# Kernel optimization log

Measured on AMD Instinct MI355X. Metric: run time of the kernel, lower is better.

The kernel has to match this reference:

```python
import jax, jax.numpy as jnp
import numpy as np


def setup_inputs() -> dict:
    key = jax.random.key(0)
    k1, k2, k3 = jax.random.split(key, 3)
    N, H, K, E = 16384, 1024, 8, 64
    x = jax.random.normal(k1, (N, H), dtype=jnp.float32)
    expert_idx = jax.random.randint(k2, (N, K), 0, E, dtype=jnp.int32)
    scale = jax.random.uniform(k3, (N,), dtype=jnp.float32)
    return {"x": x, "expert_idx": expert_idx, "scale": scale, "expert_num": E}


def reference(x, expert_idx, scale, expert_num):
    # MoE init routing v2, dropless (drop_pad_mode=0), no quant (quant_mode=0),
    # expert_tokens_num_type=0 -> cumulative counts over [0, expert_num).
    N, K = expert_idx.shape
    NK = N * K
    flat_expert = expert_idx.reshape(NK)
    # stable sort by expert id: all (token, k) slots for expert 0 first, etc.
    sort_idx = jnp.argsort(flat_expert, stable=True)          # [N*K]
    token_rows = sort_idx // K                                 # source token per expanded row
    expanded_x = x[token_rows]                                 # [N*K, H] gather
    # inverse permutation: expanded_row_idx[n*K + k] = position in expanded_x
    expanded_row_idx = jnp.zeros((NK,), dtype=jnp.int32).at[sort_idx].set(
        jnp.arange(NK, dtype=jnp.int32))
    # per-expert token counts -> cumulative sum
    counts = jax.ops.segment_sum(jnp.ones((NK,), dtype=jnp.int64),
                                 flat_expert, num_segments=expert_num)
    expert_token_cumsum = jnp.cumsum(counts)                   # [expert_num]
    expanded_scale = scale[token_rows]                         # [N*K]
    return (expanded_x, expanded_row_idx, expert_token_cumsum, expanded_scale)
```

## Files before the change

kernel.cpp:

```cpp
#include <hip/hip_runtime.h>

#define TPB 256

typedef float f32x4 __attribute__((ext_vector_type(4)));

__global__ void k_hist(const int* __restrict__ eidx, int* __restrict__ blockHist,
                       int NK, int E) {
    __shared__ int hist[256];
    int tid = threadIdx.x;
    for (int e = tid; e < E; e += TPB) hist[e] = 0;
    __syncthreads();
    int j = blockIdx.x * TPB + tid;
    if (j < NK) atomicAdd(&hist[eidx[j]], 1);
    __syncthreads();
    for (int e = tid; e < E; e += TPB)
        blockHist[(size_t)blockIdx.x * E + e] = hist[e];
}

__global__ void k_scan_blocks(int* __restrict__ blockHist, int* __restrict__ counts,
                              int numBlocks, int E) {
    __shared__ int s[TPB];
    int e = blockIdx.x;
    int tid = threadIdx.x;
    int per = (numBlocks + TPB - 1) / TPB;
    int start = tid * per;
    int end = start + per; if (end > numBlocks) end = numBlocks;
    int sum = 0;
    for (int b = start; b < end; ++b) sum += blockHist[(size_t)b * E + e];
    s[tid] = sum;
    __syncthreads();
    for (int off = 1; off < TPB; off <<= 1) {
        int t = (tid >= off) ? s[tid - off] : 0;
        __syncthreads();
        s[tid] += t;
        __syncthreads();
    }
    int run = (tid == 0) ? 0 : s[tid - 1];
    if (tid == TPB - 1) counts[e] = s[tid];
    for (int b = start; b < end; ++b) {
        size_t idx = (size_t)b * E + e;
        int v = blockHist[idx];
        blockHist[idx] = run;
        run += v;
    }
}

__global__ void k_scan_experts(const int* __restrict__ counts, int* __restrict__ offsets,
                               float* __restrict__ cumsum_out, int E) {
    if (threadIdx.x == 0) {
        int run = 0;
        for (int e = 0; e < E; ++e) {
            offsets[e] = run;
            run += counts[e];
            cumsum_out[e] = (float)run;
        }
    }
}

__global__ void k_pos(const int* __restrict__ eidx, const float* __restrict__ scale,
                      const int* __restrict__ blockHist, const int* __restrict__ offsets,
                      float* __restrict__ row_idx_out, float* __restrict__ scale_out,
                      int* __restrict__ dstPos, int NK, int E, int K) {
    __shared__ unsigned short se[TPB];
    int tid = threadIdx.x;
    int j = blockIdx.x * TPB + tid;
    int e = 0xFFFF;
    if (j < NK) e = eidx[j];
    se[tid] = (unsigned short)e;
    __syncthreads();
    if (j < NK) {
        unsigned short me = (unsigned short)e;
        int rank = 0;
        for (int t = 0; t < tid; ++t)
            rank += (se[t] == me) ? 1 : 0;
        int pos = offsets[e] + blockHist[(size_t)blockIdx.x * E + e] + rank;
        row_idx_out[j] = (float)pos;
        dstPos[j] = pos;
        scale_out[pos] = scale[j / K];
    }
}

__global__ void k_scatter(const float* __restrict__ x, const int* __restrict__ dstPos,
                          float* __restrict__ out, int H, int K, int N) {
    __shared__ int pos_s[32];
    int n4 = H >> 2;
    int tok = blockIdx.x;
    if (tok >= N) return;
    if (threadIdx.x < K) pos_s[threadIdx.x] = dstPos[tok * K + threadIdx.x];
    __syncthreads();
    const f32x4* xs = (const f32x4*)(x + (size_t)tok * H);
    for (int t = threadIdx.x; t < n4; t += blockDim.x) {
        f32x4 v = xs[t];
        #pragma unroll
        for (int k = 0; k < 8; ++k) {
            if (k < K) {
                f32x4* od = (f32x4*)(out + (size_t)pos_s[k] * H);
                __builtin_nontemporal_store(v, od + t);
            }
        }
    }
}

extern "C" void kernel_launch(void* const* d_in, const int* in_sizes, int n_in,
                              void* d_out, int out_size, void* d_ws, size_t ws_size,
                              hipStream_t stream) {
    const float* x     = (const float*)d_in[0];
    const int*   eidx  = (const int*)d_in[1];
    const float* scale = (const float*)d_in[2];

    const int N  = in_sizes[2];
    const int H  = in_sizes[0] / N;
    const int K  = in_sizes[1] / N;
    const int NK = N * K;
    const int E  = out_size - (int)((long long)NK * H) - 2 * NK;

    const int numBlocks = (NK + TPB - 1) / TPB;

    float* out_x     = (float*)d_out;
    float* out_rowix = out_x + (size_t)NK * H;
    float* out_cum   = out_rowix + NK;
    float* out_scale = out_cum + E;

    int* blockHist = (int*)d_ws;
    int* counts    = blockHist + (size_t)numBlocks * E;
    int* offsets   = counts + E;
    int* dstPos    = offsets + E;

    k_hist<<<numBlocks, TPB, 0, stream>>>(eidx, blockHist, NK, E);
    k_scan_blocks<<<E, TPB, 0, stream>>>(blockHist, counts, numBlocks, E);
    k_scan_experts<<<1, 64, 0, stream>>>(counts, offsets, out_cum, E);
    k_pos<<<numBlocks, TPB, 0, stream>>>(eidx, scale, blockHist, offsets,
                                         out_rowix, out_scale, dstPos, NK, E, K);
    k_scatter<<<N, TPB, 0, stream>>>(x, dstPos, out_x, H, K, N);
}
```

Measured before the change: 127.4 us.

## Fuse position and scatter kernels, single-block global scan, ballot-based ranking

```diff
diff --git a/kernel.cpp b/kernel.cpp
--- a/kernel.cpp
+++ b/kernel.cpp
@@ -17,85 +17,117 @@
         blockHist[(size_t)blockIdx.x * E + e] = hist[e];
 }
 
-__global__ void k_scan_blocks(int* __restrict__ blockHist, int* __restrict__ counts,
-                              int numBlocks, int E) {
-    __shared__ int s[TPB];
-    int e = blockIdx.x;
-    int tid = threadIdx.x;
-    int per = (numBlocks + TPB - 1) / TPB;
-    int start = tid * per;
-    int end = start + per; if (end > numBlocks) end = numBlocks;
+__global__ void k_scan_all(int* __restrict__ blockHist, float* __restrict__ cumsum_out,
+                           int numBlocks, int E, int CH) {
+    __shared__ int s[1024];
+    int t = threadIdx.x;
+    int nT = E * CH;
+    int e = t / CH, c = t % CH;
+    int per = (numBlocks + CH - 1) / CH;
+    int b0 = c * per;
+    int b1 = b0 + per; if (b1 > numBlocks) b1 = numBlocks;
     int sum = 0;
-    for (int b = start; b < end; ++b) sum += blockHist[(size_t)b * E + e];
-    s[tid] = sum;
+    if (t < nT)
+        for (int b = b0; b < b1; ++b) sum += blockHist[(size_t)b * E + e];
+    s[t] = (t < nT) ? sum : 0;
     __syncthreads();
-    for (int off = 1; off < TPB; off <<= 1) {
-        int t = (tid >= off) ? s[tid - off] : 0;
+    for (int off = 1; off < 1024; off <<= 1) {
+        int v = (t >= off) ? s[t - off] : 0;
         __syncthreads();
-        s[tid] += t;
+        s[t] += v;
         __syncthreads();
     }
-    int run = (tid == 0) ? 0 : s[tid - 1];
-    if (tid == TPB - 1) counts[e] = s[tid];
-    for (int b = start; b < end; ++b) {
-        size_t idx = (size_t)b * E + e;
-        int v = blockHist[idx];
-        blockHist[idx] = run;
-        run += v;
+    if (t < nT) {
+        int run = s[t] - sum;
+        for (int b = b0; b < b1; ++b) {
+            size_t idx = (size_t)b * E + e;
+            int v = blockHist[idx];
+            blockHist[idx] = run;
+            run += v;
+        }
+        if (c == CH - 1) cumsum_out[e] = (float)s[t];
     }
 }
 
-__global__ void k_scan_experts(const int* __restrict__ counts, int* __restrict__ offsets,
-                               float* __restrict__ cumsum_out, int E) {
-    if (threadIdx.x == 0) {
-        int run = 0;
-        for (int e = 0; e < E; ++e) {
-            offsets[e] = run;
-            run += counts[e];
-            cumsum_out[e] = (float)run;
+__global__ void __launch_bounds__(TPB) k_pos_scatter(
+        const int* __restrict__ eidx, const float* __restrict__ scale,
+        const int* __restrict__ blockHist, const float* __restrict__ x,
+        float* __restrict__ row_idx_out, float* __restrict__ scale_out,
+        float* __restrict__ out_x, int NK, int E, int K, int H) {
+    __shared__ int pos_sh[TPB];
+    __shared__ int whist[4 * 256];
+    __shared__ int wbase[4 * 256];
+    int tid  = threadIdx.x;
+    int j    = blockIdx.x * TPB + tid;
+    int wv   = tid >> 6;
+    int lane = tid & 63;
+
+    for (int i = tid; i < 4 * E; i += TPB) whist[i] = 0;
+    __syncthreads();
+
+    bool valid = (j < NK);
+    int e = valid ? eidx[j] : 0;
+
+    unsigned long long mask = __ballot(valid);
+    #pragma unroll
+    for (int b = 0; b < 8; ++b) {
+        unsigned long long bal = __ballot((e >> b) & 1);
+        mask &= ((e >> b) & 1) ? bal : ~bal;
+    }
+    unsigned long long lt = (1ULL << lane) - 1ULL;
+    int rank_in_wave = (int)__popcll(mask & lt);
+    bool leader = valid && ((mask & lt) == 0);
+    if (leader) whist[wv * E + e] = (int)__popcll(mask);
+    __syncthreads();
+
+    for (int ee = tid; ee < E; ee += TPB) {
+        int base = 0;
+        #pragma unroll
+        for (int w = 0; w < 4; ++w) {
+            wbase[w * E + ee] = base;
+            base += whist[w * E + ee];
         }
     }
-}
+    __syncthreads();
 
-__global__ void k_pos(const int* __restrict__ eidx, const float* __restrict__ scale,
-                      const int* __restrict__ blockHist, const int* __restrict__ offsets,
-                      float* __restrict__ row_idx_out, float* __restrict__ scale_out,
-                      int* __restrict__ dstPos, int NK, int E, int K) {
-    __shared__ unsigned short se[TPB];
-    int tid = threadIdx.x;
-    int j = blockIdx.x * TPB + tid;
-    int e = 0xFFFF;
-    if (j < NK) e = eidx[j];
-    se[tid] = (unsigned short)e;
+    if (valid) {
+        int pos = blockHist[(size_t)blockIdx.x * E + e] + wbase[wv * E + e] + rank_in_wave;
+        row_idx_out[j] = (float)pos;
+        scale_out[pos] = scale[j / K];
+        pos_sh[tid] = pos;
+    }
     __syncthreads();
-    if (j < NK) {
-        unsigned short me = (unsigned short)e;
-        int rank = 0;
-        for (int t = 0; t < tid; ++t)
-            rank += (se[t] == me) ? 1 : 0;
-        int pos = offsets[e] + blockHist[(size_t)blockIdx.x * E + e] + rank;
-        row_idx_out[j] = (float)pos;
-        dstPos[j] = pos;
-        scale_out[pos] = scale[j / K];
-    }
-}
 
-__global__ void k_scatter(const float* __restrict__ x, const int* __restrict__ dstPos,
-                          float* __restrict__ out, int H, int K, int N) {
-    __shared__ int pos_s[32];
+    int tpb_tok = TPB / K;
+    int tok0 = blockIdx.x * tpb_tok;
     int n4 = H >> 2;
-    int tok = blockIdx.x;
-    if (tok >= N) return;
-    if (threadIdx.x < K) pos_s[threadIdx.x] = dstPos[tok * K + threadIdx.x];
-    __syncthreads();
-    const f32x4* xs = (const f32x4*)(x + (size_t)tok * H);
-    for (int t = threadIdx.x; t < n4; t += blockDim.x) {
-        f32x4 v = xs[t];
-        #pragma unroll
-        for (int k = 0; k < 8; ++k) {
-            if (k < K) {
-                f32x4* od = (f32x4*)(out + (size_t)pos_s[k] * H);
-                __builtin_nontemporal_store(v, od + t);
+    for (int tl = 0; tl < tpb_tok; ++tl) {
+        int tok = tok0 + tl;
+        if ((size_t)tok * K >= (size_t)NK) break;
+        const f32x4* xs = (const f32x4*)(x + (size_t)tok * H);
+        if (K == 8) {
+            int p0 = pos_sh[tl * 8 + 0], p1 = pos_sh[tl * 8 + 1];
+            int p2 = pos_sh[tl * 8 + 2], p3 = pos_sh[tl * 8 + 3];
+            int p4 = pos_sh[tl * 8 + 4], p5 = pos_sh[tl * 8 + 5];
+            int p6 = pos_sh[tl * 8 + 6], p7 = pos_sh[tl * 8 + 7];
+            for (int t = tid; t < n4; t += TPB) {
+                f32x4 v = xs[t];
+                __builtin_nontemporal_store(v, (f32x4*)(out_x + (size_t)p0 * H) + t);
+                __builtin_nontemporal_store(v, (f32x4*)(out_x + (size_t)p1 * H) + t);
+                __builtin_nontemporal_store(v, (f32x4*)(out_x + (size_t)p2 * H) + t);
+                __builtin_nontemporal_store(v, (f32x4*)(out_x + (size_t)p3 * H) + t);
+                __builtin_nontemporal_store(v, (f32x4*)(out_x + (size_t)p4 * H) + t);
+                __builtin_nontemporal_store(v, (f32x4*)(out_x + (size_t)p5 * H) + t);
+                __builtin_nontemporal_store(v, (f32x4*)(out_x + (size_t)p6 * H) + t);
+                __builtin_nontemporal_store(v, (f32x4*)(out_x + (size_t)p7 * H) + t);
+            }
+        } else {
+            for (int t = tid; t < n4; t += TPB) {
+                f32x4 v = xs[t];
+                for (int k = 0; k < K; ++k) {
+                    f32x4* od = (f32x4*)(out_x + (size_t)pos_sh[tl * K + k] * H);
+                    __builtin_nontemporal_store(v, od + t);
+                }
             }
         }
     }
@@ -122,14 +154,12 @@
     float* out_scale = out_cum + E;
 
     int* blockHist = (int*)d_ws;
-    int* counts    = blockHist + (size_t)numBlocks * E;
-    int* offsets   = counts + E;
-    int* dstPos    = offsets + E;
+
+    int CH = 1024 / E; if (CH < 1) CH = 1;
 
     k_hist<<<numBlocks, TPB, 0, stream>>>(eidx, blockHist, NK, E);
-    k_scan_blocks<<<E, TPB, 0, stream>>>(blockHist, counts, numBlocks, E);
-    k_scan_experts<<<1, 64, 0, stream>>>(counts, offsets, out_cum, E);
-    k_pos<<<numBlocks, TPB, 0, stream>>>(eidx, scale, blockHist, offsets,
-                                         out_rowix, out_scale, dstPos, NK, E, K);
-    k_scatter<<<N, TPB, 0, stream>>>(x, dstPos, out_x, H, K, N);
+    k_scan_all<<<1, 1024, 0, stream>>>(blockHist, out_cum, numBlocks, E, CH);
+    k_pos_scatter<<<numBlocks, TPB, 0, stream>>>(eidx, scale, blockHist, x,
+                                                 out_rowix, out_scale, out_x,
+                                                 NK, E, K, H);
 }
```

After: 154.4 us. 1.21x slower.

## Replace quadratic in-block rank loop with wave ballot match and per-wave histograms

Applied to the files above, without the earlier changes.

```diff
diff --git a/kernel.cpp b/kernel.cpp
--- a/kernel.cpp
+++ b/kernel.cpp
@@ -57,23 +57,49 @@
     }
 }
 
-__global__ void k_pos(const int* __restrict__ eidx, const float* __restrict__ scale,
-                      const int* __restrict__ blockHist, const int* __restrict__ offsets,
-                      float* __restrict__ row_idx_out, float* __restrict__ scale_out,
-                      int* __restrict__ dstPos, int NK, int E, int K) {
-    __shared__ unsigned short se[TPB];
-    int tid = threadIdx.x;
-    int j = blockIdx.x * TPB + tid;
-    int e = 0xFFFF;
-    if (j < NK) e = eidx[j];
-    se[tid] = (unsigned short)e;
+__global__ void __launch_bounds__(TPB) k_pos(
+        const int* __restrict__ eidx, const float* __restrict__ scale,
+        const int* __restrict__ blockHist, const int* __restrict__ offsets,
+        float* __restrict__ row_idx_out, float* __restrict__ scale_out,
+        int* __restrict__ dstPos, int NK, int E, int K) {
+    __shared__ int whist[4 * 256];
+    __shared__ int wbase[4 * 256];
+    int tid  = threadIdx.x;
+    int j    = blockIdx.x * TPB + tid;
+    int wv   = tid >> 6;
+    int lane = tid & 63;
+
+    for (int i = tid; i < 4 * E; i += TPB) whist[i] = 0;
     __syncthreads();
-    if (j < NK) {
-        unsigned short me = (unsigned short)e;
-        int rank = 0;
-        for (int t = 0; t < tid; ++t)
-            rank += (se[t] == me) ? 1 : 0;
-        int pos = offsets[e] + blockHist[(size_t)blockIdx.x * E + e] + rank;
+
+    bool valid = (j < NK);
+    int e = valid ? eidx[j] : 0;
+
+    unsigned long long mask = __ballot(valid);
+    #pragma unroll
+    for (int b = 0; b < 8; ++b) {
+        unsigned long long bal = __ballot((e >> b) & 1);
+        mask &= ((e >> b) & 1) ? bal : ~bal;
+    }
+    unsigned long long lt = (1ULL << lane) - 1ULL;
+    int rank_in_wave = (int)__popcll(mask & lt);
+    bool leader = valid && ((mask & lt) == 0);
+    if (leader) whist[wv * E + e] = (int)__popcll(mask);
+    __syncthreads();
+
+    for (int ee = tid; ee < E; ee += TPB) {
+        int base = 0;
+        #pragma unroll
+        for (int w = 0; w < 4; ++w) {
+            wbase[w * E + ee] = base;
+            base += whist[w * E + ee];
+        }
+    }
+    __syncthreads();
+
+    if (valid) {
+        int pos = offsets[e] + blockHist[(size_t)blockIdx.x * E + e]
+                + wbase[wv * E + e] + rank_in_wave;
         row_idx_out[j] = (float)pos;
         dstPos[j] = pos;
         scale_out[pos] = scale[j / K];
@@ -90,7 +116,7 @@
     __syncthreads();
     const f32x4* xs = (const f32x4*)(x + (size_t)tok * H);
     for (int t = threadIdx.x; t < n4; t += blockDim.x) {
-        f32x4 v = xs[t];
+        f32x4 v = __builtin_nontemporal_load(xs + t);
         #pragma unroll
         for (int k = 0; k < 8; ++k) {
             if (k < K) {
```

Measured after the change: 142.9 us. 12.2% more time.

## Fuse position computation and scatter into one wave-per-token kernel with ballot ranking

Applied to the files above, without the earlier changes.

```diff
diff --git a/kernel.cpp b/kernel.cpp
--- a/kernel.cpp
+++ b/kernel.cpp
@@ -4,27 +4,30 @@
 
 typedef float f32x4 __attribute__((ext_vector_type(4)));
 
+
 __global__ void k_hist(const int* __restrict__ eidx, int* __restrict__ blockHist,
                        int NK, int E) {
-    __shared__ int hist[256];
+    __shared__ int hist[4 * 64];
     int tid = threadIdx.x;
-    for (int e = tid; e < E; e += TPB) hist[e] = 0;
+    int wv = tid >> 6, lane = tid & 63;
+    hist[tid & 255] = 0;
     __syncthreads();
     int j = blockIdx.x * TPB + tid;
-    if (j < NK) atomicAdd(&hist[eidx[j]], 1);
+    if (j < NK) atomicAdd(&hist[wv * 64 + eidx[j]], 1);
     __syncthreads();
-    for (int e = tid; e < E; e += TPB)
-        blockHist[(size_t)blockIdx.x * E + e] = hist[e];
+    int c = blockIdx.x * 4 + wv;
+    if (lane < E && (size_t)c * 64 < (size_t)NK)
+        blockHist[(size_t)c * E + lane] = hist[wv * 64 + lane];
 }
 
 __global__ void k_scan_blocks(int* __restrict__ blockHist, int* __restrict__ counts,
-                              int numBlocks, int E) {
+                              int numChunks, int E) {
     __shared__ int s[TPB];
     int e = blockIdx.x;
     int tid = threadIdx.x;
-    int per = (numBlocks + TPB - 1) / TPB;
+    int per = (numChunks + TPB - 1) / TPB;
     int start = tid * per;
-    int end = start + per; if (end > numBlocks) end = numBlocks;
+    int end = start + per; if (end > numChunks) end = numChunks;
     int sum = 0;
     for (int b = start; b < end; ++b) sum += blockHist[(size_t)b * E + e];
     s[tid] = sum;
@@ -45,59 +48,84 @@
     }
 }
 
-__global__ void k_scan_experts(const int* __restrict__ counts, int* __restrict__ offsets,
-                               float* __restrict__ cumsum_out, int E) {
-    if (threadIdx.x == 0) {
-        int run = 0;
-        for (int e = 0; e < E; ++e) {
-            offsets[e] = run;
-            run += counts[e];
-            cumsum_out[e] = (float)run;
+__global__ void __launch_bounds__(TPB) k_pos_scatter(
+        const int* __restrict__ eidx, const float* __restrict__ scale,
+        const int* __restrict__ blockHist, const int* __restrict__ counts,
+        const float* __restrict__ x,
+        float* __restrict__ row_idx_out, float* __restrict__ scale_out,
+        float* __restrict__ cumsum_out, float* __restrict__ out_x,
+        int NK, int E, int K, int H, int N) {
+    int tid  = threadIdx.x;
+    int wv   = tid >> 6;
+    int lane = tid & 63;
+    int tok  = blockIdx.x * 4 + wv;
+    if (tok >= N) return;
+    int spw  = 64 / K;
+    int c    = tok / spw;
+    int s    = tok - c * spw;
+
+    const f32x4* xs = (const f32x4*)(x + (size_t)tok * H);
+    int n4 = H >> 2;
+    f32x4 v0, v1, v2, v3;
+    if (lane       < n4) v0 = xs[lane];
+    if (lane + 64  < n4) v1 = xs[lane + 64];
+    if (lane + 128 < n4) v2 = xs[lane + 128];
+    if (lane + 192 < n4) v3 = xs[lane + 192];
+
+    int j = c * 64 + lane;
+    bool valid = (j < NK);
+    int ei = valid ? eidx[j] : 0;
+
+    unsigned long long mask = __ballot(valid);
+    #pragma unroll
+    for (int b = 0; b < 6; ++b) {
+        unsigned long long bal = __ballot((ei >> b) & 1);
+        mask &= ((ei >> b) & 1) ? bal : ~bal;
+    }
+    unsigned long long lt = (1ULL << lane) - 1ULL;
+    int rank = (int)__popcll(mask & lt);
+
+    int bh = (lane < E) ? blockHist[(size_t)c * E + lane] : 0;
+    int base_e = __shfl(bh, ei);
+
+    int cnt = (lane < E) ? counts[lane] : 0;
+    int inc = cnt;
+    #pragma unroll
+    for (int off = 1; off < 64; off <<= 1) {
+        int v = __shfl_up(inc, off);
+        if (lane >= off) inc += v;
+    }
+    int off_e = __shfl(inc - cnt, ei);
+
+    int pos = off_e + base_e + rank;
+
+    if (tok == 0 && lane < E) cumsum_out[lane] = (float)inc;
+
+    if (s == 0 && valid) {
+        row_idx_out[j] = (float)pos;
+        scale_out[pos] = scale[j / K];
+    }
+
+    int pk[8];
+    #pragma unroll
+    for (int k = 0; k < 8; ++k)
+        if (k < K) pk[k] = __shfl(pos, s * K + k);
+
+    #pragma unroll
+    for (int k = 0; k < 8; ++k) {
+        if (k < K) {
+            f32x4* od = (f32x4*)(out_x + (size_t)pk[k] * H);
+            if (lane       < n4) __builtin_nontemporal_store(v0, od + lane);
+            if (lane + 64  < n4) __builtin_nontemporal_store(v1, od + lane + 64);
+            if (lane + 128 < n4) __builtin_nontemporal_store(v2, od + lane + 128);
+            if (lane + 192 < n4) __builtin_nontemporal_store(v3, od + lane + 192);
         }
     }
-}
-
-__global__ void k_pos(const int* __restrict__ eidx, const float* __restrict__ scale,
-                      const int* __restrict__ blockHist, const int* __restrict__ offsets,
-                      float* __restrict__ row_idx_out, float* __restrict__ scale_out,
-                      int* __restrict__ dstPos, int NK, int E, int K) {
-    __shared__ unsigned short se[TPB];
-    int tid = threadIdx.x;
-    int j = blockIdx.x * TPB + tid;
-    int e = 0xFFFF;
-    if (j < NK) e = eidx[j];
-    se[tid] = (unsigned short)e;
-    __syncthreads();
-    if (j < NK) {
-        unsigned short me = (unsigned short)e;
-        int rank = 0;
-        for (int t = 0; t < tid; ++t)
-            rank += (se[t] == me) ? 1 : 0;
-        int pos = offsets[e] + blockHist[(size_t)blockIdx.x * E + e] + rank;
-        row_idx_out[j] = (float)pos;
-        dstPos[j] = pos;
-        scale_out[pos] = scale[j / K];
-    }
-}
-
-__global__ void k_scatter(const float* __restrict__ x, const int* __restrict__ dstPos,
-                          float* __restrict__ out, int H, int K, int N) {
-    __shared__ int pos_s[32];
-    int n4 = H >> 2;
-    int tok = blockIdx.x;
-    if (tok >= N) return;
-    if (threadIdx.x < K) pos_s[threadIdx.x] = dstPos[tok * K + threadIdx.x];
-    __syncthreads();
-    const f32x4* xs = (const f32x4*)(x + (size_t)tok * H);
-    for (int t = threadIdx.x; t < n4; t += blockDim.x) {
+    for (int t = lane + 256; t < n4; t += 64) {
         f32x4 v = xs[t];
         #pragma unroll
-        for (int k = 0; k < 8; ++k) {
-            if (k < K) {
-                f32x4* od = (f32x4*)(out + (size_t)pos_s[k] * H);
-                __builtin_nontemporal_store(v, od + t);
-            }
-        }
+        for (int k = 0; k < 8; ++k)
+            if (k < K) __builtin_nontemporal_store(v, (f32x4*)(out_x + (size_t)pk[k] * H) + t);
     }
 }
 
@@ -114,7 +142,8 @@
     const int NK = N * K;
     const int E  = out_size - (int)((long long)NK * H) - 2 * NK;
 
-    const int numBlocks = (NK + TPB - 1) / TPB;
+    const int numChunks = (NK + 63) / 64;
+    const int histBlocks = (NK + TPB - 1) / TPB;
 
     float* out_x     = (float*)d_out;
     float* out_rowix = out_x + (size_t)NK * H;
@@ -122,14 +151,11 @@
     float* out_scale = out_cum + E;
 
     int* blockHist = (int*)d_ws;
-    int* counts    = blockHist + (size_t)numBlocks * E;
-    int* offsets   = counts + E;
-    int* dstPos    = offsets + E;
+    int* counts    = blockHist + (size_t)numChunks * E;
 
-    k_hist<<<numBlocks, TPB, 0, stream>>>(eidx, blockHist, NK, E);
-    k_scan_blocks<<<E, TPB, 0, stream>>>(blockHist, counts, numBlocks, E);
-    k_scan_experts<<<1, 64, 0, stream>>>(counts, offsets, out_cum, E);
-    k_pos<<<numBlocks, TPB, 0, stream>>>(eidx, scale, blockHist, offsets,
-                                         out_rowix, out_scale, dstPos, NK, E, K);
-    k_scatter<<<N, TPB, 0, stream>>>(x, dstPos, out_x, H, K, N);
+    k_hist<<<histBlocks, TPB, 0, stream>>>(eidx, blockHist, NK, E);
+    k_scan_blocks<<<E, TPB, 0, stream>>>(blockHist, counts, numChunks, E);
+    k_pos_scatter<<<(N + 3) / 4, TPB, 0, stream>>>(eidx, scale, blockHist, counts, x,
+                                                   out_rowix, out_scale, out_cum, out_x,
+                                                   NK, E, K, H, N);
 }
```

Result: no change. 126.0 us (-1.1%).
